# Kernel tuning notes

Measured on AMD Instinct MI355X. Metric: run time of the kernel, lower is better.

## Reference

```python
import jax, jax.numpy as jnp
import numpy as np

B, L, D_MODEL, N_HEADS = 2, 2048, 2048, 16
HALF = D_MODEL // 2            # 1024
HD = HALF // N_HEADS           # 64 (head dim actually used by the reshape)
SCALE = float(np.sqrt(D_MODEL / N_HEADS))  # sqrt(128), per source's self.scale
EPS = 1e-5


def setup_inputs() -> dict:
    key = jax.random.key(0)
    ks = jax.random.split(key, 12)
    s = 1.0 / np.sqrt(HALF)
    d = dict(
        x_a=jax.random.normal(ks[0], (B, L, HALF), jnp.float32),
        x_b=jax.random.normal(ks[1], (B, L, HALF), jnp.float32),
        Wq_a=jax.random.normal(ks[2], (HALF, HALF), jnp.float32) * s,
        Wq_b=jax.random.normal(ks[3], (HALF, HALF), jnp.float32) * s,
        Wk_a=jax.random.normal(ks[4], (HALF, HALF), jnp.float32) * s,
        Wk_b=jax.random.normal(ks[5], (HALF, HALF), jnp.float32) * s,
        Wv_a=jax.random.normal(ks[6], (HALF, HALF), jnp.float32) * s,
        Wv_b=jax.random.normal(ks[7], (HALF, HALF), jnp.float32) * s,
        Wo_a=jax.random.normal(ks[8], (HALF, HALF), jnp.float32) * s,
        Wo_b=jax.random.normal(ks[9], (HALF, HALF), jnp.float32) * s,
        gamma_a=jnp.ones((HALF,), jnp.float32),
        beta_a=jnp.zeros((HALF,), jnp.float32),
        gamma_b=jnp.ones((HALF,), jnp.float32),
        beta_b=jnp.zeros((HALF,), jnp.float32),
    )
    return d


def _heads(x, W):
    # torch Linear (no bias): x @ W.T, then split heads -> (B, H, L, HD)
    y = jnp.einsum('bld,ed->ble', x, W)
    Bb, Ll, _ = y.shape
    return y.reshape(Bb, Ll, N_HEADS, HD).transpose(0, 2, 1, 3)


def _ln(x, gamma, beta):
    mu = jnp.mean(x, axis=-1, keepdims=True)
    var = jnp.var(x, axis=-1, keepdims=True)
    return (x - mu) * jax.lax.rsqrt(var + EPS) * gamma + beta


def reference(x_a, x_b, Wq_a, Wq_b, Wk_a, Wk_b, Wv_a, Wv_b, Wo_a, Wo_b,
              gamma_a, beta_a, gamma_b, beta_b):
    q_a = _heads(x_a, Wq_a); k_a = _heads(x_a, Wk_a); v_a = _heads(x_a, Wv_a)
    q_b = _heads(x_b, Wq_b); k_b = _heads(x_b, Wk_b); v_b = _heads(x_b, Wv_b)

    # cross-attention: branch a attends over branch b and vice versa
    scores_a = jnp.einsum('bhqd,bhkd->bhqk', q_a, k_b) / SCALE
    scores_b = jnp.einsum('bhqd,bhkd->bhqk', q_b, k_a) / SCALE
    w_a = jax.nn.softmax(scores_a, axis=-1)
    w_b = jax.nn.softmax(scores_b, axis=-1)

    o_a = jnp.einsum('bhqk,bhkd->bhqd', w_a, v_b)
    o_b = jnp.einsum('bhqk,bhkd->bhqd', w_b, v_a)
    o_a = o_a.transpose(0, 2, 1, 3).reshape(x_a.shape)
    o_b = o_b.transpose(0, 2, 1, 3).reshape(x_b.shape)

    o_a = jnp.einsum('bld,ed->ble', o_a, Wo_a)
    o_b = jnp.einsum('bld,ed->ble', o_b, Wo_b)

    y_a = _ln(x_a + o_a, gamma_a, beta_a)
    y_b = _ln(x_b + o_b, gamma_b, beta_b)
    return y_a, y_b
```

## Files before the change

### kernel.cpp

```cpp
#include <hip/hip_runtime.h>
#include <cstdint>
#include <cstddef>

typedef __bf16 bf16x8 __attribute__((ext_vector_type(8)));
typedef float f32x4 __attribute__((ext_vector_type(4)));
typedef unsigned short u16x8 __attribute__((ext_vector_type(8)));
typedef unsigned short u16x4 __attribute__((ext_vector_type(4)));
typedef short s16x4 __attribute__((ext_vector_type(4)));
typedef unsigned short u16;

#define L_SEQ 2048
#define D_HALF 1024
#define HDIM 64
static constexpr float EXP2_SCALE = 0.12751742552639395f;

__device__ inline u16 f2b(float f) {
  uint32_t u; __builtin_memcpy(&u, &f, 4);
  u = u + 0x7FFFu + ((u >> 16) & 1u);
  return (u16)(u >> 16);
}

__device__ inline uint32_t cvt_pk_bf16(float lo, float hi) {
  uint32_t r;
  asm("v_cvt_pk_bf16_f32 %0, %1, %2" : "=v"(r) : "v"(lo), "v"(hi));
  return r;
}

#define GLOAD16(gp, lp) __builtin_amdgcn_global_load_lds( \
    (const __attribute__((address_space(1))) unsigned int*)(gp), \
    (__attribute__((address_space(3))) unsigned int*)(lp), 16, 0, 0)

__global__ __launch_bounds__(256)
void convx(const float* xa, const float* xb, u16* dst) {
  const float* s = blockIdx.y ? xb : xa;
  size_t i = ((size_t)blockIdx.x * 256 + threadIdx.x) * 8;
  float4 v0 = *(const float4*)(s + i);
  float4 v1 = *(const float4*)(s + i + 4);
  u16x8 p;
  p[0] = f2b(v0.x); p[1] = f2b(v0.y); p[2] = f2b(v0.z); p[3] = f2b(v0.w);
  p[4] = f2b(v1.x); p[5] = f2b(v1.y); p[6] = f2b(v1.z); p[7] = f2b(v1.w);
  *(u16x8*)&dst[(size_t)blockIdx.y * 4194304 + i] = p;
}

struct CArg8 { const float* src[8]; };
__global__ __launch_bounds__(256)
void convw8(CArg8 a, u16* dst) {
  const int z = blockIdx.y;
  const float* s = a.src[z];
  size_t i = ((size_t)blockIdx.x * 256 + threadIdx.x) * 8;
  float4 v0 = *(const float4*)(s + i);
  float4 v1 = *(const float4*)(s + i + 4);
  u16x8 p;
  p[0] = f2b(v0.x); p[1] = f2b(v0.y); p[2] = f2b(v0.z); p[3] = f2b(v0.w);
  p[4] = f2b(v1.x); p[5] = f2b(v1.y); p[6] = f2b(v1.z); p[7] = f2b(v1.w);
  *(u16x8*)&dst[(size_t)z * 1048576 + i] = p;
}

struct GArg { const u16* A; const u16* W; u16* C; const float* R; float* Z;
              int vt; float alpha; };
struct GArgs { GArg g[6]; };

template <bool RESID>
__global__ __launch_bounds__(256, 2)
void gemm_nt(GArgs args, int M, int N, int K) {
  GArg ga = args.g[blockIdx.z];
  __shared__ __attribute__((aligned(16))) u16 As[2][8192];
  __shared__ __attribute__((aligned(16))) u16 Bs[2][8192];

  const int tid = threadIdx.x;
  const int wv = tid >> 6, lane = tid & 63;
  const int lane15 = lane & 15, quad = lane >> 4;
  const int m0 = blockIdx.y * 128, n0 = blockIdx.x * 128;
  const int wm = (wv >> 1) * 64, wn = (wv & 1) * 64;

  const int srow = lane >> 3;
  const int scol = ((lane & 7) ^ srow) * 8;

  const u16* pA[4]; const u16* pW[4]; int lo[4];
#pragma unroll
  for (int j = 0; j < 4; j++) {
    int r = wv * 32 + j * 8;
    pA[j] = ga.A + (size_t)(m0 + r + srow) * K + scol;
    pW[j] = ga.W + (size_t)(n0 + r + srow) * K + scol;
    lo[j] = r * 64;
  }

  f32x4 acc[4][4] = {};
  const int swz = (lane15 & 7) << 4;

#pragma unroll
  for (int j = 0; j < 4; j++) {
    GLOAD16(pA[j], &As[0][lo[j]]);
    GLOAD16(pW[j], &Bs[0][lo[j]]);
  }

  for (int k0 = 0; k0 < K; k0 += 64) {
    const int cur = (k0 >> 6) & 1;
    __syncthreads();
    if (k0 + 64 < K) {
#pragma unroll
      for (int j = 0; j < 4; j++) {
        GLOAD16(pA[j] + k0 + 64, &As[cur ^ 1][lo[j]]);
        GLOAD16(pW[j] + k0 + 64, &Bs[cur ^ 1][lo[j]]);
      }
    }
    const char* ab = (const char*)As[cur];
    const char* bb = (const char*)Bs[cur];
#pragma unroll
    for (int kk = 0; kk < 2; kk++) {
      const int cb = kk * 64 + quad * 16;
      bf16x8 af[4], bw[4];
#pragma unroll
      for (int i = 0; i < 4; i++)
        af[i] = *(const bf16x8*)(ab + (wm + i * 16 + lane15) * 128 + (cb ^ swz));
#pragma unroll
      for (int j = 0; j < 4; j++)
        bw[j] = *(const bf16x8*)(bb + (wn + j * 16 + lane15) * 128 + (cb ^ swz));
#pragma unroll
      for (int i = 0; i < 4; i++)
#pragma unroll
        for (int j = 0; j < 4; j++)
          acc[i][j] = __builtin_amdgcn_mfma_f32_16x16x32_bf16(af[i], bw[j], acc[i][j], 0, 0, 0);
    }
  }

  const float al = ga.alpha;
  if (!RESID && ga.vt) {
#pragma unroll
    for (int i = 0; i < 4; i++)
#pragma unroll
      for (int j = 0; j < 4; j++) {
        int gm0 = m0 + wm + i * 16 + quad * 4;
        int gn  = n0 + wn + j * 16 + lane15;
        int bb2 = gm0 >> 11, t = gm0 & 2047;
        u16x4 pk;
#pragma unroll
        for (int r = 0; r < 4; r++) pk[r] = f2b(acc[i][j][r] * al);
        *(u16x4*)&ga.C[(size_t)bb2 * 2097152 + (size_t)gn * 2048 + t] = pk;
      }
  } else {
#pragma unroll
    for (int i = 0; i < 4; i++)
#pragma unroll
      for (int j = 0; j < 4; j++)
#pragma unroll
        for (int r = 0; r < 4; r++) {
          int gm = m0 + wm + i * 16 + quad * 4 + r;
          int gn = n0 + wn + j * 16 + lane15;
          size_t idx = (size_t)gm * N + gn;
          if (RESID) ga.Z[idx] = acc[i][j][r] + ga.R[idx];
          else       ga.C[idx] = f2b(acc[i][j][r] * al);
        }
  }
}

#define SWZ(row, bcol) ((row) * 128 + ((bcol) ^ (((row) & 7) << 4)))

__global__ __launch_bounds__(256, 2)
void attn_kernel(const u16* q_a, const u16* k_a, const u16* vt_a,
                 const u16* q_b, const u16* k_b, const u16* vt_b,
                 u16* o_a, u16* o_b) {
  const int br = blockIdx.z;
  const u16* Q  = br ? q_b : q_a;
  const u16* Kp = br ? k_a : k_b;
  const u16* Vp = br ? vt_a : vt_b;
  u16* O = br ? o_b : o_a;
  const int bh = blockIdx.y;
  const int b = bh >> 4, h = bh & 15;
  const int q0 = blockIdx.x * 128;

  const int tid = threadIdx.x, wv = tid >> 6, lane = tid & 63;
  const int lane15 = lane & 15, quad = lane >> 4;

  __shared__ __attribute__((aligned(16))) u16 Ks[2][4096];
  __shared__ __attribute__((aligned(16))) u16 Vt[2][4096];

  const size_t base   = ((size_t)b * L_SEQ) * D_HALF + (size_t)h * HDIM;
  const size_t vbase  = (size_t)b * 2097152 + (size_t)(h * 64) * 2048;

  const int c1 = tid + 256;
  const int r0 = tid >> 3, cb0 = (tid & 7) * 16;
  const int r1 = c1 >> 3,  cb1 = (c1 & 7) * 16;
  const int wo0 = SWZ(r0, cb0), wo1 = SWZ(r1, cb1);

  bf16x8 qf[2][2];
#pragma unroll
  for (int f = 0; f < 2; f++) {
    const int qrow = q0 + wv * 32 + f * 16 + lane15;
#pragma unroll
    for (int c = 0; c < 2; c++)
      qf[f][c] = *(const bf16x8*)&Q[base + (size_t)qrow * D_HALF + c * 32 + quad * 8];
  }

  u16x8 kr0 = *(const u16x8*)&Kp[base + (size_t)r0 * D_HALF + cb0 / 2];
  u16x8 kr1 = *(const u16x8*)&Kp[base + (size_t)r1 * D_HALF + cb1 / 2];
  u16x8 vr0 = *(const u16x8*)&Vp[vbase + (size_t)r0 * 2048 + cb0 / 2];
  u16x8 vr1 = *(const u16x8*)&Vp[vbase + (size_t)r1 * 2048 + cb1 / 2];
  *(u16x8*)((char*)Ks[0] + wo0) = kr0;
  *(u16x8*)((char*)Ks[0] + wo1) = kr1;
  *(u16x8*)((char*)Vt[0] + wo0) = vr0;
  *(u16x8*)((char*)Vt[0] + wo1) = vr1;
  __syncthreads();

  f32x4 oacc[2][4] = {};
  float lsum[2] = {0.f, 0.f};
  const int aswz = (lane15 & 7) << 4;

  for (int it = 0; it < 32; it++) {
    const int cur = it & 1, nxt = cur ^ 1;
    if (it < 31) {
      const int kt = (it + 1) * 64;
      kr0 = *(const u16x8*)&Kp[base + (size_t)(kt + r0) * D_HALF + cb0 / 2];
      kr1 = *(const u16x8*)&Kp[base + (size_t)(kt + r1) * D_HALF + cb1 / 2];
      vr0 = *(const u16x8*)&Vp[vbase + (size_t)r0 * 2048 + kt + cb0 / 2];
      vr1 = *(const u16x8*)&Vp[vbase + (size_t)r1 * 2048 + kt + cb1 / 2];
    }

    const char* kb = (const char*)Ks[cur];
    const char* vb = (const char*)Vt[cur];

    f32x4 s[2][4];
    __builtin_amdgcn_s_setprio(1);
#pragma unroll
    for (int nt = 0; nt < 4; nt++) {
      const int krow = nt * 16 + lane15;
      bf16x8 kb0 = *(const bf16x8*)(kb + SWZ(krow, quad * 16));
      bf16x8 kb1 = *(const bf16x8*)(kb + SWZ(krow, 64 + quad * 16));
#pragma unroll
      for (int f = 0; f < 2; f++) {
        f32x4 a0 = {};
        a0 = __builtin_amdgcn_mfma_f32_16x16x32_bf16(kb0, qf[f][0], a0, 0, 0, 0);
        a0 = __builtin_amdgcn_mfma_f32_16x16x32_bf16(kb1, qf[f][1], a0, 0, 0, 0);
        s[f][nt] = a0;
      }
    }
    __builtin_amdgcn_s_setprio(0);

    s16x4 pa[2][4];
#pragma unroll
    for (int f = 0; f < 2; f++)
#pragma unroll
      for (int nt = 0; nt < 4; nt++) {
        float p0 = __builtin_amdgcn_exp2f(s[f][nt][0]);
        float p1 = __builtin_amdgcn_exp2f(s[f][nt][1]);
        float p2 = __builtin_amdgcn_exp2f(s[f][nt][2]);
        float p3 = __builtin_amdgcn_exp2f(s[f][nt][3]);
        lsum[f] += (p0 + p1) + (p2 + p3);
        union { uint32_t u[2]; s16x4 v; } cv;
        cv.u[0] = cvt_pk_bf16(p0, p1);
        cv.u[1] = cvt_pk_bf16(p2, p3);
        pa[f][nt] = cv.v;
      }

    __builtin_amdgcn_s_setprio(1);
#pragma unroll
    for (int dt = 0; dt < 4; dt++) {
      const int vrow = dt * 16 + lane15;
      s16x4 bv[4];
#pragma unroll
      for (int nt = 0; nt < 4; nt++)
        bv[nt] = *(const s16x4*)(vb + SWZ(vrow, nt * 32 + quad * 8));
#pragma unroll
      for (int f = 0; f < 2; f++) {
        f32x4 t = oacc[f][dt];
#pragma unroll
        for (int nt = 0; nt < 4; nt++)
          t = __builtin_amdgcn_mfma_f32_16x16x16bf16_1k(pa[f][nt], bv[nt], t, 0, 0, 0);
        oacc[f][dt] = t;
      }
    }
    __builtin_amdgcn_s_setprio(0);

    if (it < 31) {
      *(u16x8*)((char*)Ks[nxt] + wo0) = kr0;
      *(u16x8*)((char*)Ks[nxt] + wo1) = kr1;
      *(u16x8*)((char*)Vt[nxt] + wo0) = vr0;
      *(u16x8*)((char*)Vt[nxt] + wo1) = vr1;
    }
    __syncthreads();
  }

#pragma unroll
  for (int f = 0; f < 2; f++) {
    float lt = lsum[f];
    lt += __shfl_xor(lt, 16);
    lt += __shfl_xor(lt, 32);
    lsum[f] = lt;
  }
#pragma unroll
  for (int f = 0; f < 2; f++) {
    float linv[4];
#pragma unroll
    for (int r = 0; r < 4; r++)
      linv[r] = 1.0f / __shfl(lsum[f], quad * 4 + r);
#pragma unroll
    for (int dt = 0; dt < 4; dt++)
#pragma unroll
      for (int r = 0; r < 4; r++) {
        float val = oacc[f][dt][r] * linv[r];
        O[base + (size_t)(q0 + wv * 32 + f * 16 + quad * 4 + r) * D_HALF
          + dt * 16 + lane15] = f2b(val);
      }
  }
}

__global__ __launch_bounds__(256)
void ln_kernel(const float* zA, const float* zB,
               const float* gA, const float* bA, const float* gB, const float* bB,
               float* out) {
  const int row = blockIdx.x, br = blockIdx.y;
  const float* z = (br ? zB : zA) + (size_t)row * D_HALF;
  const float* g  = br ? gB : gA;
  const float* be = br ? bB : bA;
  float* o = out + (size_t)br * ((size_t)4096 * D_HALF) + (size_t)row * D_HALF;

  float4 v = ((const float4*)z)[threadIdx.x];
  float s  = v.x + v.y + v.z + v.w;
  float s2 = v.x * v.x + v.y * v.y + v.z * v.z + v.w * v.w;
#pragma unroll
  for (int off = 32; off > 0; off >>= 1) {
    s  += __shfl_down(s, off);
    s2 += __shfl_down(s2, off);
  }
  __shared__ float red[8];
  int w = threadIdx.x >> 6, ln = threadIdx.x & 63;
  if (ln == 0) { red[w] = s; red[4 + w] = s2; }
  __syncthreads();
  if (threadIdx.x == 0) {
    red[0] = red[0] + red[1] + red[2] + red[3];
    red[4] = red[4] + red[5] + red[6] + red[7];
  }
  __syncthreads();
  float mu  = red[0] * (1.0f / 1024.0f);
  float var = red[4] * (1.0f / 1024.0f) - mu * mu;
  float rs  = rsqrtf(fmaxf(var, 0.0f) + 1e-5f);

  int col = threadIdx.x * 4;
  float4 gv = ((const float4*)g)[threadIdx.x];
  float4 bv = ((const float4*)be)[threadIdx.x];
  float4 ov;
  ov.x = (v.x - mu) * rs * gv.x + bv.x;
  ov.y = (v.y - mu) * rs * gv.y + bv.y;
  ov.z = (v.z - mu) * rs * gv.z + bv.z;
  ov.w = (v.w - mu) * rs * gv.w + bv.w;
  *(float4*)&o[col] = ov;
}

extern "C" void kernel_launch(void* const* d_in, const int* in_sizes, int n_in,
                              void* d_out, int out_size, void* d_ws, size_t ws_size,
                              hipStream_t stream) {
  const float* x_a     = (const float*)d_in[0];
  const float* x_b     = (const float*)d_in[1];
  const float* Wq_a    = (const float*)d_in[2];
  const float* Wq_b    = (const float*)d_in[3];
  const float* Wk_a    = (const float*)d_in[4];
  const float* Wk_b    = (const float*)d_in[5];
  const float* Wv_a    = (const float*)d_in[6];
  const float* Wv_b    = (const float*)d_in[7];
  const float* Wo_a    = (const float*)d_in[8];
  const float* Wo_b    = (const float*)d_in[9];
  const float* gamma_a = (const float*)d_in[10];
  const float* beta_a  = (const float*)d_in[11];
  const float* gamma_b = (const float*)d_in[12];
  const float* beta_b  = (const float*)d_in[13];

  const size_t BUF = (size_t)4096 * 1024;
  u16* ws   = (u16*)d_ws;
  u16* q_a  = ws + 0 * BUF; u16* k_a  = ws + 1 * BUF; u16* vt_a = ws + 2 * BUF;
  u16* q_b  = ws + 3 * BUF; u16* k_b  = ws + 4 * BUF; u16* vt_b = ws + 5 * BUF;
  u16* wall = ws + 6 * BUF;
  float* z_a = (float*)(ws + 0 * BUF);
  float* z_b = (float*)(ws + 2 * BUF);

  u16* xbf_a = (u16*)d_out;
  u16* xbf_b = xbf_a + 4194304;
  u16* o_a   = (u16*)d_out;
  u16* o_b   = o_a + 4194304;

  const int M = 4096, N = 1024, K = 1024;

  convx<<<dim3(2048, 2), 256, 0, stream>>>(x_a, x_b, xbf_a);

  CArg8 cw;
  cw.src[0] = Wq_a; cw.src[1] = Wk_a; cw.src[2] = Wv_a;
  cw.src[3] = Wq_b; cw.src[4] = Wk_b; cw.src[5] = Wv_b;
  cw.src[6] = Wo_a; cw.src[7] = Wo_b;
  convw8<<<dim3(512, 8), 256, 0, stream>>>(cw, wall);

  GArgs qkv;
  qkv.g[0] = GArg{xbf_a, wall + 0 * 1048576, q_a,  nullptr, nullptr, 0, EXP2_SCALE};
  qkv.g[1] = GArg{xbf_a, wall + 1 * 1048576, k_a,  nullptr, nullptr, 0, 1.0f};
  qkv.g[2] = GArg{xbf_a, wall + 2 * 1048576, vt_a, nullptr, nullptr, 1, 1.0f};
  qkv.g[3] = GArg{xbf_b, wall + 3 * 1048576, q_b,  nullptr, nullptr, 0, EXP2_SCALE};
  qkv.g[4] = GArg{xbf_b, wall + 4 * 1048576, k_b,  nullptr, nullptr, 0, 1.0f};
  qkv.g[5] = GArg{xbf_b, wall + 5 * 1048576, vt_b, nullptr, nullptr, 1, 1.0f};
  gemm_nt<false><<<dim3(8, 32, 6), 256, 0, stream>>>(qkv, M, N, K);

  attn_kernel<<<dim3(16, 32, 2), 256, 0, stream>>>(q_a, k_a, vt_a, q_b, k_b, vt_b, o_a, o_b);

  GArgs op;
  op.g[0] = GArg{o_a, wall + 6 * 1048576, nullptr, x_a, z_a, 0, 1.0f};
  op.g[1] = GArg{o_b, wall + 7 * 1048576, nullptr, x_b, z_b, 0, 1.0f};
  op.g[2] = op.g[0]; op.g[3] = op.g[0]; op.g[4] = op.g[0]; op.g[5] = op.g[0];
  gemm_nt<true><<<dim3(8, 32, 2), 256, 0, stream>>>(op, M, N, K);

  ln_kernel<<<dim3(4096, 2), 256, 0, stream>>>(z_a, z_b, gamma_a, beta_a,
                                               gamma_b, beta_b, (float*)d_out);
}
```

Baseline: 340.3 us.

## Software-pipeline attention QK^T one tile ahead; single-buffer GEMM LDS

The attention kernel now computes the QK^T scores for the next key tile before the softmax and PV of the current tile. It also preloads the V fragments into registers and issues the global prefetch two tiles ahead, so MFMA work can overlap the exp computation and global loads. The GEMM drops its LDS double buffering in favour of a single buffer with load-then-sync each K step. Both kernels lose the min-blocks-per-CU=2 launch bound, which allows more registers per thread but may reduce occupancy; the GEMM change removes load/compute overlap and risks exposing global latency.

```diff
diff --git a/kernel.cpp b/kernel.cpp
--- a/kernel.cpp
+++ b/kernel.cpp
@@ -61,11 +61,11 @@
 struct GArgs { GArg g[6]; };
 
 template <bool RESID>
-__global__ __launch_bounds__(256, 2)
+__global__ __launch_bounds__(256)
 void gemm_nt(GArgs args, int M, int N, int K) {
   GArg ga = args.g[blockIdx.z];
-  __shared__ __attribute__((aligned(16))) u16 As[2][8192];
-  __shared__ __attribute__((aligned(16))) u16 Bs[2][8192];
+  __shared__ __attribute__((aligned(16))) u16 As[8192];
+  __shared__ __attribute__((aligned(16))) u16 Bs[8192];
 
   const int tid = threadIdx.x;
   const int wv = tid >> 6, lane = tid & 63;
@@ -88,24 +88,16 @@
   f32x4 acc[4][4] = {};
   const int swz = (lane15 & 7) << 4;
 
-#pragma unroll
-  for (int j = 0; j < 4; j++) {
-    GLOAD16(pA[j], &As[0][lo[j]]);
-    GLOAD16(pW[j], &Bs[0][lo[j]]);
-  }
-
   for (int k0 = 0; k0 < K; k0 += 64) {
-    const int cur = (k0 >> 6) & 1;
     __syncthreads();
-    if (k0 + 64 < K) {
-#pragma unroll
-      for (int j = 0; j < 4; j++) {
-        GLOAD16(pA[j] + k0 + 64, &As[cur ^ 1][lo[j]]);
-        GLOAD16(pW[j] + k0 + 64, &Bs[cur ^ 1][lo[j]]);
-      }
-    }
-    const char* ab = (const char*)As[cur];
-    const char* bb = (const char*)Bs[cur];
+#pragma unroll
+    for (int j = 0; j < 4; j++) {
+      GLOAD16(pA[j] + k0, &As[lo[j]]);
+      GLOAD16(pW[j] + k0, &Bs[lo[j]]);
+    }
+    __syncthreads();
+    const char* ab = (const char*)As;
+    const char* bb = (const char*)Bs;
 #pragma unroll
     for (int kk = 0; kk < 2; kk++) {
       const int cb = kk * 64 + quad * 16;
@@ -156,7 +148,7 @@
 
 #define SWZ(row, bcol) ((row) * 128 + ((bcol) ^ (((row) & 7) << 4)))
 
-__global__ __launch_bounds__(256, 2)
+__global__ __launch_bounds__(256)
 void attn_kernel(const u16* q_a, const u16* k_a, const u16* vt_a,
                  const u16* q_b, const u16* k_b, const u16* vt_b,
                  u16* o_a, u16* o_b) {
@@ -202,25 +194,14 @@
   *(u16x8*)((char*)Vt[0] + wo1) = vr1;
   __syncthreads();
 
-  f32x4 oacc[2][4] = {};
-  float lsum[2] = {0.f, 0.f};
-  const int aswz = (lane15 & 7) << 4;
-
-  for (int it = 0; it < 32; it++) {
-    const int cur = it & 1, nxt = cur ^ 1;
-    if (it < 31) {
-      const int kt = (it + 1) * 64;
-      kr0 = *(const u16x8*)&Kp[base + (size_t)(kt + r0) * D_HALF + cb0 / 2];
-      kr1 = *(const u16x8*)&Kp[base + (size_t)(kt + r1) * D_HALF + cb1 / 2];
-      vr0 = *(const u16x8*)&Vp[vbase + (size_t)r0 * 2048 + kt + cb0 / 2];
-      vr1 = *(const u16x8*)&Vp[vbase + (size_t)r1 * 2048 + kt + cb1 / 2];
-    }
-
-    const char* kb = (const char*)Ks[cur];
-    const char* vb = (const char*)Vt[cur];
-
-    f32x4 s[2][4];
-    __builtin_amdgcn_s_setprio(1);
+  kr0 = *(const u16x8*)&Kp[base + (size_t)(64 + r0) * D_HALF + cb0 / 2];
+  kr1 = *(const u16x8*)&Kp[base + (size_t)(64 + r1) * D_HALF + cb1 / 2];
+  vr0 = *(const u16x8*)&Vp[vbase + (size_t)r0 * 2048 + 64 + cb0 / 2];
+  vr1 = *(const u16x8*)&Vp[vbase + (size_t)r1 * 2048 + 64 + cb1 / 2];
+
+  f32x4 s_cur[2][4];
+  {
+    const char* kb = (const char*)Ks[0];
 #pragma unroll
     for (int nt = 0; nt < 4; nt++) {
       const int krow = nt * 16 + lane15;
@@ -231,20 +212,71 @@
         f32x4 a0 = {};
         a0 = __builtin_amdgcn_mfma_f32_16x16x32_bf16(kb0, qf[f][0], a0, 0, 0, 0);
         a0 = __builtin_amdgcn_mfma_f32_16x16x32_bf16(kb1, qf[f][1], a0, 0, 0, 0);
-        s[f][nt] = a0;
-      }
-    }
-    __builtin_amdgcn_s_setprio(0);
+        s_cur[f][nt] = a0;
+      }
+    }
+  }
+  s16x4 vf[4][4];
+  {
+    const char* vb = (const char*)Vt[0];
+#pragma unroll
+    for (int dt = 0; dt < 4; dt++)
+#pragma unroll
+      for (int nt = 0; nt < 4; nt++)
+        vf[dt][nt] = *(const s16x4*)(vb + SWZ(dt * 16 + lane15, nt * 32 + quad * 8));
+  }
+
+  f32x4 oacc[2][4] = {};
+  float lsum[2] = {0.f, 0.f};
+
+#pragma unroll 2
+  for (int it = 0; it < 32; it++) {
+    const int nxtb = (it + 1) & 1;
+    char* kn = (char*)Ks[nxtb];
+    char* vn = (char*)Vt[nxtb];
+    if (it < 31) {
+      *(u16x8*)(kn + wo0) = kr0;
+      *(u16x8*)(kn + wo1) = kr1;
+      *(u16x8*)(vn + wo0) = vr0;
+      *(u16x8*)(vn + wo1) = vr1;
+    }
+    __syncthreads();
+
+    f32x4 s_nx[2][4];
+    if (it < 31) {
+      __builtin_amdgcn_s_setprio(1);
+#pragma unroll
+      for (int nt = 0; nt < 4; nt++) {
+        const int krow = nt * 16 + lane15;
+        bf16x8 kb0 = *(const bf16x8*)(kn + SWZ(krow, quad * 16));
+        bf16x8 kb1 = *(const bf16x8*)(kn + SWZ(krow, 64 + quad * 16));
+#pragma unroll
+        for (int f = 0; f < 2; f++) {
+          f32x4 a0 = {};
+          a0 = __builtin_amdgcn_mfma_f32_16x16x32_bf16(kb0, qf[f][0], a0, 0, 0, 0);
+          a0 = __builtin_amdgcn_mfma_f32_16x16x32_bf16(kb1, qf[f][1], a0, 0, 0, 0);
+          s_nx[f][nt] = a0;
+        }
+      }
+      __builtin_amdgcn_s_setprio(0);
+      if (it < 30) {
+        const int kt = (it + 2) * 64;
+        kr0 = *(const u16x8*)&Kp[base + (size_t)(kt + r0) * D_HALF + cb0 / 2];
+        kr1 = *(const u16x8*)&Kp[base + (size_t)(kt + r1) * D_HALF + cb1 / 2];
+        vr0 = *(const u16x8*)&Vp[vbase + (size_t)r0 * 2048 + kt + cb0 / 2];
+        vr1 = *(const u16x8*)&Vp[vbase + (size_t)r1 * 2048 + kt + cb1 / 2];
+      }
+    }
 
     s16x4 pa[2][4];
 #pragma unroll
     for (int f = 0; f < 2; f++)
 #pragma unroll
       for (int nt = 0; nt < 4; nt++) {
-        float p0 = __builtin_amdgcn_exp2f(s[f][nt][0]);
-        float p1 = __builtin_amdgcn_exp2f(s[f][nt][1]);
-        float p2 = __builtin_amdgcn_exp2f(s[f][nt][2]);
-        float p3 = __builtin_amdgcn_exp2f(s[f][nt][3]);
+        float p0 = __builtin_amdgcn_exp2f(s_cur[f][nt][0]);
+        float p1 = __builtin_amdgcn_exp2f(s_cur[f][nt][1]);
+        float p2 = __builtin_amdgcn_exp2f(s_cur[f][nt][2]);
+        float p3 = __builtin_amdgcn_exp2f(s_cur[f][nt][3]);
         lsum[f] += (p0 + p1) + (p2 + p3);
         union { uint32_t u[2]; s16x4 v; } cv;
         cv.u[0] = cvt_pk_bf16(p0, p1);
@@ -254,30 +286,29 @@
 
     __builtin_amdgcn_s_setprio(1);
 #pragma unroll
-    for (int dt = 0; dt < 4; dt++) {
-      const int vrow = dt * 16 + lane15;
-      s16x4 bv[4];
-#pragma unroll
-      for (int nt = 0; nt < 4; nt++)
-        bv[nt] = *(const s16x4*)(vb + SWZ(vrow, nt * 32 + quad * 8));
+    for (int dt = 0; dt < 4; dt++)
 #pragma unroll
       for (int f = 0; f < 2; f++) {
         f32x4 t = oacc[f][dt];
 #pragma unroll
         for (int nt = 0; nt < 4; nt++)
-          t = __builtin_amdgcn_mfma_f32_16x16x16bf16_1k(pa[f][nt], bv[nt], t, 0, 0, 0);
+          t = __builtin_amdgcn_mfma_f32_16x16x16bf16_1k(pa[f][nt], vf[dt][nt], t, 0, 0, 0);
         oacc[f][dt] = t;
       }
-    }
     __builtin_amdgcn_s_setprio(0);
 
     if (it < 31) {
-      *(u16x8*)((char*)Ks[nxt] + wo0) = kr0;
-      *(u16x8*)((char*)Ks[nxt] + wo1) = kr1;
-      *(u16x8*)((char*)Vt[nxt] + wo0) = vr0;
-      *(u16x8*)((char*)Vt[nxt] + wo1) = vr1;
-    }
-    __syncthreads();
+#pragma unroll
+      for (int dt = 0; dt < 4; dt++)
+#pragma unroll
+        for (int nt = 0; nt < 4; nt++)
+          vf[dt][nt] = *(const s16x4*)(vn + SWZ(dt * 16 + lane15, nt * 32 + quad * 8));
+#pragma unroll
+      for (int f = 0; f < 2; f++)
+#pragma unroll
+        for (int nt = 0; nt < 4; nt++)
+          s_cur[f][nt] = s_nx[f][nt];
+    }
   }
 
 #pragma unroll
```

New measurement: 376.9 us. 1.11x slower.

## Deepen GEMM prefetch with explicit vmcnt waits and merge conversion kernels

Applied to the files above, without the earlier changes.

Restructures the GEMM main loop so two K-tiles are in flight. Each loop step waits with s_waitcnt vmcnt and raw s_barrier instead of __syncthreads, letting loads for tile t+2 overlap compute on tile t+1. It also fuses the activation and weight fp32-to-bf16 conversion kernels into one launch, and drops the min-blocks-per-CU launch bound. The extra barriers and manual waitcnt add sync complexity, and removing the occupancy hint may change register allocation.

```diff
diff --git a/kernel.cpp b/kernel.cpp
--- a/kernel.cpp
+++ b/kernel.cpp
@@ -30,30 +30,20 @@
     (const __attribute__((address_space(1))) unsigned int*)(gp), \
     (__attribute__((address_space(3))) unsigned int*)(lp), 16, 0, 0)
 
+struct CArgAll { const float* src[10]; u16* dst[10]; };
 __global__ __launch_bounds__(256)
-void convx(const float* xa, const float* xb, u16* dst) {
-  const float* s = blockIdx.y ? xb : xa;
-  size_t i = ((size_t)blockIdx.x * 256 + threadIdx.x) * 8;
+void convall(CArgAll a) {
+  const int id = blockIdx.x;
+  const float* s; u16* d; int blk;
+  if (id < 4096) { int p = id >> 11; blk = id & 2047; s = a.src[p]; d = a.dst[p]; }
+  else { int w = (id - 4096) >> 9; blk = (id - 4096) & 511; s = a.src[2 + w]; d = a.dst[2 + w]; }
+  size_t i = ((size_t)blk * 256 + threadIdx.x) * 8;
   float4 v0 = *(const float4*)(s + i);
   float4 v1 = *(const float4*)(s + i + 4);
   u16x8 p;
   p[0] = f2b(v0.x); p[1] = f2b(v0.y); p[2] = f2b(v0.z); p[3] = f2b(v0.w);
   p[4] = f2b(v1.x); p[5] = f2b(v1.y); p[6] = f2b(v1.z); p[7] = f2b(v1.w);
-  *(u16x8*)&dst[(size_t)blockIdx.y * 4194304 + i] = p;
-}
-
-struct CArg8 { const float* src[8]; };
-__global__ __launch_bounds__(256)
-void convw8(CArg8 a, u16* dst) {
-  const int z = blockIdx.y;
-  const float* s = a.src[z];
-  size_t i = ((size_t)blockIdx.x * 256 + threadIdx.x) * 8;
-  float4 v0 = *(const float4*)(s + i);
-  float4 v1 = *(const float4*)(s + i + 4);
-  u16x8 p;
-  p[0] = f2b(v0.x); p[1] = f2b(v0.y); p[2] = f2b(v0.z); p[3] = f2b(v0.w);
-  p[4] = f2b(v1.x); p[5] = f2b(v1.y); p[6] = f2b(v1.z); p[7] = f2b(v1.w);
-  *(u16x8*)&dst[(size_t)z * 1048576 + i] = p;
+  *(u16x8*)&d[i] = p;
 }
 
 struct GArg { const u16* A; const u16* W; u16* C; const float* R; float* Z;
@@ -61,7 +51,7 @@
 struct GArgs { GArg g[6]; };
 
 template <bool RESID>
-__global__ __launch_bounds__(256, 2)
+__global__ __launch_bounds__(256)
 void gemm_nt(GArgs args, int M, int N, int K) {
   GArg ga = args.g[blockIdx.z];
   __shared__ __attribute__((aligned(16))) u16 As[2][8192];
@@ -87,23 +77,24 @@
 
   f32x4 acc[4][4] = {};
   const int swz = (lane15 & 7) << 4;
+  const int NT = K >> 6;
 
 #pragma unroll
   for (int j = 0; j < 4; j++) {
     GLOAD16(pA[j], &As[0][lo[j]]);
     GLOAD16(pW[j], &Bs[0][lo[j]]);
   }
-
-  for (int k0 = 0; k0 < K; k0 += 64) {
-    const int cur = (k0 >> 6) & 1;
-    __syncthreads();
-    if (k0 + 64 < K) {
-#pragma unroll
-      for (int j = 0; j < 4; j++) {
-        GLOAD16(pA[j] + k0 + 64, &As[cur ^ 1][lo[j]]);
-        GLOAD16(pW[j] + k0 + 64, &Bs[cur ^ 1][lo[j]]);
-      }
-    }
+#pragma unroll
+  for (int j = 0; j < 4; j++) {
+    GLOAD16(pA[j] + 64, &As[1][lo[j]]);
+    GLOAD16(pW[j] + 64, &Bs[1][lo[j]]);
+  }
+  asm volatile("s_waitcnt vmcnt(8)" ::: "memory");
+  __builtin_amdgcn_s_barrier();
+  __builtin_amdgcn_sched_barrier(0);
+
+  for (int t = 0; t < NT; ++t) {
+    const int cur = t & 1;
     const char* ab = (const char*)As[cur];
     const char* bb = (const char*)Bs[cur];
 #pragma unroll
@@ -122,6 +113,23 @@
         for (int j = 0; j < 4; j++)
           acc[i][j] = __builtin_amdgcn_mfma_f32_16x16x32_bf16(af[i], bw[j], acc[i][j], 0, 0, 0);
     }
+    __builtin_amdgcn_sched_barrier(0);
+    __builtin_amdgcn_s_barrier();
+    __builtin_amdgcn_sched_barrier(0);
+    if (t + 2 < NT) {
+#pragma unroll
+      for (int j = 0; j < 4; j++) {
+        GLOAD16(pA[j] + (size_t)(t + 2) * 64, &As[cur][lo[j]]);
+        GLOAD16(pW[j] + (size_t)(t + 2) * 64, &Bs[cur][lo[j]]);
+      }
+      asm volatile("s_waitcnt vmcnt(8)" ::: "memory");
+    } else if (t + 1 < NT) {
+      asm volatile("s_waitcnt vmcnt(0)" ::: "memory");
+    }
+    if (t + 1 < NT) {
+      __builtin_amdgcn_s_barrier();
+      __builtin_amdgcn_sched_barrier(0);
+    }
   }
 
   const float al = ga.alpha;
@@ -132,11 +140,11 @@
       for (int j = 0; j < 4; j++) {
         int gm0 = m0 + wm + i * 16 + quad * 4;
         int gn  = n0 + wn + j * 16 + lane15;
-        int bb2 = gm0 >> 11, t = gm0 & 2047;
+        int bb2 = gm0 >> 11, tt = gm0 & 2047;
         u16x4 pk;
 #pragma unroll
         for (int r = 0; r < 4; r++) pk[r] = f2b(acc[i][j][r] * al);
-        *(u16x4*)&ga.C[(size_t)bb2 * 2097152 + (size_t)gn * 2048 + t] = pk;
+        *(u16x4*)&ga.C[(size_t)bb2 * 2097152 + (size_t)gn * 2048 + tt] = pk;
       }
   } else {
 #pragma unroll
@@ -204,7 +212,6 @@
 
   f32x4 oacc[2][4] = {};
   float lsum[2] = {0.f, 0.f};
-  const int aswz = (lane15 & 7) << 4;
 
   for (int it = 0; it < 32; it++) {
     const int cur = it & 1, nxt = cur ^ 1;
@@ -379,13 +386,14 @@
 
   const int M = 4096, N = 1024, K = 1024;
 
-  convx<<<dim3(2048, 2), 256, 0, stream>>>(x_a, x_b, xbf_a);
-
-  CArg8 cw;
-  cw.src[0] = Wq_a; cw.src[1] = Wk_a; cw.src[2] = Wv_a;
-  cw.src[3] = Wq_b; cw.src[4] = Wk_b; cw.src[5] = Wv_b;
-  cw.src[6] = Wo_a; cw.src[7] = Wo_b;
-  convw8<<<dim3(512, 8), 256, 0, stream>>>(cw, wall);
+  CArgAll ca;
+  ca.src[0] = x_a;  ca.dst[0] = xbf_a;
+  ca.src[1] = x_b;  ca.dst[1] = xbf_b;
+  ca.src[2] = Wq_a; ca.src[3] = Wk_a; ca.src[4] = Wv_a;
+  ca.src[5] = Wq_b; ca.src[6] = Wk_b; ca.src[7] = Wv_b;
+  ca.src[8] = Wo_a; ca.src[9] = Wo_b;
+  for (int w = 0; w < 8; w++) ca.dst[2 + w] = wall + (size_t)w * 1048576;
+  convall<<<dim3(8192), 256, 0, stream>>>(ca);
 
   GArgs qkv;
   qkv.g[0] = GArg{xbf_a, wall + 0 * 1048576, q_a,  nullptr, nullptr, 0, EXP2_SCALE};
```

Result: no change. 342.0 us (+0.5%).
